# Kernel optimization log

Measured on AMD Instinct MI355X. Metric: run time of the kernel, lower is better.

The kernel has to match this reference:

```python
import jax, jax.numpy as jnp
import numpy as np

NUM_HEADS = 8


def setup_inputs() -> dict:
    key = jax.random.key(0)
    k1, k2, k3 = jax.random.split(key, 3)
    B, N, C = 4, 2048, 1024
    x = jax.random.normal(k1, (B, N, C), dtype=jnp.float32)
    # torch nn.Linear layout: [out_features, in_features]; scaled for stability
    Wqkv = jax.random.normal(k2, (3 * C, C), dtype=jnp.float32) * (C ** -0.5)
    Wproj = jax.random.normal(k3, (C, C), dtype=jnp.float32) * (C ** -0.5)
    return {"x": x, "Wqkv": Wqkv, "Wproj": Wproj}


def reference(x, Wqkv, Wproj):
    B, N, C = x.shape
    H = NUM_HEADS
    D = C // H
    # fused QKV projection (bias=False per config)
    qkv = jnp.einsum('bnc,oc->bno', x, Wqkv)          # [B, N, 3C]
    qkv = qkv.reshape(B, N, 3, H, D)
    q = jnp.transpose(qkv[:, :, 0], (0, 2, 1, 3))     # [B, H, N, D]
    k = jnp.transpose(qkv[:, :, 1], (0, 2, 1, 3))
    v = jnp.transpose(qkv[:, :, 2], (0, 2, 1, 3))
    scale = 1.0 / jnp.sqrt(jnp.asarray(D, dtype=x.dtype))
    scores = jnp.einsum('bhqd,bhkd->bhqk', q, k) * scale
    attn = jax.nn.softmax(scores, axis=-1)            # attn_drop is identity (p=0)
    out = jnp.einsum('bhqk,bhkd->bhqd', attn, v)      # [B, H, N, D]
    out = jnp.transpose(out, (0, 2, 1, 3)).reshape(B, N, C)
    out = jnp.einsum('bnc,oc->bno', out, Wproj)       # proj_drop is identity (p=0)
    return out
```

## Files before the change

### kernel.cpp

```cpp
#include <hip/hip_runtime.h>
#include <hip/hip_bf16.h>
#include <stdint.h>


typedef __bf16 bf16x8 __attribute__((ext_vector_type(8)));
typedef float  f32x4  __attribute__((ext_vector_type(4)));
typedef float  f32x16 __attribute__((ext_vector_type(16)));
typedef short  s16x8  __attribute__((ext_vector_type(8)));
typedef unsigned int u32x4 __attribute__((ext_vector_type(4)));

__device__ __forceinline__ f32x4 mfma_bf16(s16x8 a, s16x8 b, f32x4 c) {
  return __builtin_amdgcn_mfma_f32_16x16x32_bf16(
      __builtin_bit_cast(bf16x8, a), __builtin_bit_cast(bf16x8, b), c, 0, 0, 0);
}

__device__ __forceinline__ f32x16 mfma32(s16x8 a, s16x8 b, f32x16 c) {
  return __builtin_amdgcn_mfma_f32_32x32x16_bf16(
      __builtin_bit_cast(bf16x8, a), __builtin_bit_cast(bf16x8, b), c, 0, 0, 0);
}

__device__ __forceinline__ unsigned short f2bf(float f) {
  unsigned u = __float_as_uint(f);
  u = u + 0x7FFFu + ((u >> 16) & 1u);
  return (unsigned short)(u >> 16);
}

__device__ __forceinline__ unsigned cvt_pk_bf16(float lo, float hi) {
  unsigned r;
  asm("v_cvt_pk_bf16_f32 %0, %1, %2" : "=v"(r) : "v"(lo), "v"(hi));
  return r;
}

__device__ __forceinline__ void load_lds16(const void* g, void* l) {
  __builtin_amdgcn_global_load_lds(
      (const __attribute__((address_space(1))) void*)g,
      (__attribute__((address_space(3))) void*)l, 16, 0, 0);
}


__global__ void cast_kernel(const float* __restrict__ in,
                            unsigned short* __restrict__ out, int n4) {
  int i = blockIdx.x * blockDim.x + threadIdx.x;
  int stride = gridDim.x * blockDim.x;
  for (; i < n4; i += stride) {
    float4 v = reinterpret_cast<const float4*>(in)[i];
    ushort4 o;
    o.x = f2bf(v.x); o.y = f2bf(v.y); o.z = f2bf(v.z); o.w = f2bf(v.w);
    reinterpret_cast<ushort4*>(out)[i] = o;
  }
}


template <bool OUT_BF16>
__global__ __launch_bounds__(256)
void gemm_bt(const short* __restrict__ A, const short* __restrict__ Bw,
             void* __restrict__ Cp, int M, int N, int K) {
  __shared__ __align__(16) short lds_a[4096];
  __shared__ __align__(16) short lds_b[4096];

  const int nbn = N >> 7;
  const int mb  = blockIdx.x / nbn;
  const int nb  = blockIdx.x % nbn;
  const int tid = threadIdx.x;
  const int w   = tid >> 6, l = tid & 63;
  const int lg  = l >> 4, ll = l & 15;
  const int wm  = w >> 1, wn = w & 1;

  f32x4 acc[4][4];
#pragma unroll
  for (int i = 0; i < 4; ++i)
#pragma unroll
    for (int j = 0; j < 4; ++j) acc[i][j] = {0.f, 0.f, 0.f, 0.f};

  const int KT = K >> 5;
  for (int kt = 0; kt < KT; ++kt) {
#pragma unroll
    for (int cc = 0; cc < 4; ++cc) {
      int chunk = w * 4 + cc;
      int c8    = chunk & 7;
      int row   = c8 * 16 + (l >> 2);
      int sg    = (l & 3) ^ (row & 3);
      if (chunk < 8) {
        const short* src = A + (size_t)(mb * 128 + row) * K + kt * 32 + sg * 8;
        load_lds16(src, lds_a + c8 * 512);
      } else {
        const short* src = Bw + (size_t)(nb * 128 + row) * K + kt * 32 + sg * 8;
        load_lds16(src, lds_b + c8 * 512);
      }
    }
    __syncthreads();

    s16x8 af[4], bf[4];
#pragma unroll
    for (int mi = 0; mi < 4; ++mi) {
      int row  = wm * 64 + mi * 16 + ll;
      int slot = lg ^ (row & 3);
      af[mi] = *reinterpret_cast<const s16x8*>(lds_a + row * 32 + slot * 8);
    }
#pragma unroll
    for (int nj = 0; nj < 4; ++nj) {
      int row  = wn * 64 + nj * 16 + ll;
      int slot = lg ^ (row & 3);
      bf[nj] = *reinterpret_cast<const s16x8*>(lds_b + row * 32 + slot * 8);
    }
#pragma unroll
    for (int mi = 0; mi < 4; ++mi)
#pragma unroll
      for (int nj = 0; nj < 4; ++nj)
        acc[mi][nj] = mfma_bf16(af[mi], bf[nj], acc[mi][nj]);
    __syncthreads();
  }

#pragma unroll
  for (int mi = 0; mi < 4; ++mi) {
#pragma unroll
    for (int i = 0; i < 4; ++i) {
      size_t row = (size_t)(mb * 128 + wm * 64 + mi * 16 + lg * 4 + i);
#pragma unroll
      for (int nj = 0; nj < 4; ++nj) {
        int col = nb * 128 + wn * 64 + nj * 16 + ll;
        if (OUT_BF16)
          ((unsigned short*)Cp)[row * N + col] = f2bf(acc[mi][nj][i]);
        else
          ((float*)Cp)[row * N + col] = acc[mi][nj][i];
      }
    }
  }
}


__global__ __launch_bounds__(512, 2)
void attn_fwd(const short* __restrict__ qkv, unsigned short* __restrict__ aout) {
  __shared__ __align__(16) short k_lds[2][64 * 128];
  __shared__ __align__(16) short v_lds[2][128 * 64];

  const int bh = blockIdx.x >> 3;
  const int qb = blockIdx.x & 7;
  const int b = bh >> 3, h = bh & 7;
  const int tid = threadIdx.x;
  const int w = tid >> 6, l = tid & 63;
  const int col = l & 31, hi = l >> 5;

  const size_t base = (size_t)b * 2048 * 3072 + (size_t)h * 128;
  const int qrow0 = qb * 256 + w * 32;

  s16x8 qf[8];
  {
    const short* qp = qkv + base + (size_t)(qrow0 + col) * 3072 + hi * 8;
#pragma unroll
    for (int ks = 0; ks < 8; ++ks)
      qf[ks] = *reinterpret_cast<const s16x8*>(qp + ks * 16);
  }

  f32x16 oacc[4];
#pragma unroll
  for (int nt = 0; nt < 4; ++nt)
#pragma unroll
    for (int r = 0; r < 16; ++r) oacc[nt][r] = 0.f;
  float M = -1e30f, L = 0.f;
  const float csc = 0.08838834764831845f * 1.4426950408889634f;

  s16x8 vr0a, vr0b, vr1a, vr1b;
  const int vr_r0 = (tid & 31) * 2;
  const int vr_c0 = ((tid >> 5) & 7) * 16;

  auto stage_k = [&](int kb, int bf) {
    int wk = w - 4;
#pragma unroll
    for (int cc = 0; cc < 4; ++cc) {
      int c = wk * 4 + cc;
      int row = c * 4 + (l >> 4);
      int sd = (l & 15) ^ (row & 7);
      load_lds16(qkv + base + 1024 + (size_t)(kb * 64 + row) * 3072 + sd * 8,
                 &k_lds[bf][c * 512]);
    }
  };
  auto load_v = [&](int kb) {
    const short* g = qkv + base + 2048 + (size_t)(kb * 64 + vr_r0) * 3072 + vr_c0;
    vr0a = *reinterpret_cast<const s16x8*>(g);
    vr0b = *reinterpret_cast<const s16x8*>(g + 8);
    vr1a = *reinterpret_cast<const s16x8*>(g + 3072);
    vr1b = *reinterpret_cast<const s16x8*>(g + 3072 + 8);
  };
  auto write_v = [&](int bf) {
    char* vbase = reinterpret_cast<char*>(v_lds[bf]);
#pragma unroll
    for (int j = 0; j < 16; ++j) {
      int d = vr_c0 + j;
      unsigned e0 = (unsigned short)(j < 8 ? vr0a[j] : vr0b[j - 8]);
      unsigned e1 = (unsigned short)(j < 8 ? vr1a[j] : vr1b[j - 8]);
      int byte = d * 128 + ((((vr_r0 * 2) >> 4) ^ (d & 7)) << 4) + ((vr_r0 * 2) & 15);
      *reinterpret_cast<unsigned*>(vbase + byte) = e0 | (e1 << 16);
    }
  };

  if (w >= 4) stage_k(0, 0);
  else { load_v(0); write_v(0); }
  __syncthreads();

  for (int kb = 0; kb < 32; ++kb) {
    const int bf = kb & 1;
    if (kb < 31) {
      if (w >= 4) stage_k(kb + 1, bf ^ 1);
      else load_v(kb + 1);
    }

    f32x16 st[2];
#pragma unroll
    for (int kt = 0; kt < 2; ++kt)
#pragma unroll
      for (int r = 0; r < 16; ++r) st[kt][r] = 0.f;
    const char* kbase = reinterpret_cast<const char*>(k_lds[bf]);
#pragma unroll
    for (int ks = 0; ks < 8; ++ks) {
#pragma unroll
      for (int kt = 0; kt < 2; ++kt) {
        int krow = kt * 32 + col;
        int slot = (ks * 2 + hi) ^ (krow & 7);
        s16x8 ak = *reinterpret_cast<const s16x8*>(kbase + krow * 256 + slot * 16);
        st[kt] = mfma32(ak, qf[ks], st[kt]);
      }
    }

    float pm = st[0][0];
#pragma unroll
    for (int r = 1; r < 16; ++r) pm = fmaxf(pm, st[0][r]);
#pragma unroll
    for (int r = 0; r < 16; ++r) pm = fmaxf(pm, st[1][r]);
    pm *= csc;
    pm = fmaxf(pm, __shfl_xor(pm, 32));
    if (!__all(pm <= M + 8.0f)) {
      float Mn = fmaxf(M, pm);
      float f = exp2f(M - Mn);
      M = Mn; L *= f;
#pragma unroll
      for (int r = 0; r < 16; ++r) {
        float fr = __shfl(f, (r & 3) + 8 * (r >> 2) + 4 * hi);
#pragma unroll
        for (int nt = 0; nt < 4; ++nt) oacc[nt][r] *= fr;
      }
    }
    float rs = 0.f;
#pragma unroll
    for (int kt = 0; kt < 2; ++kt)
#pragma unroll
      for (int r = 0; r < 16; ++r) {
        float e = exp2f(fmaf(st[kt][r], csc, -M));
        st[kt][r] = e;
        rs += e;
      }
    rs += __shfl_xor(rs, 32);
    L += rs;

    unsigned wd[16], pw[16];
#pragma unroll
    for (int i = 0; i < 8; ++i) {
      wd[i]     = cvt_pk_bf16(st[0][2 * i], st[0][2 * i + 1]);
      wd[8 + i] = cvt_pk_bf16(st[1][2 * i], st[1][2 * i + 1]);
    }
#pragma unroll
    for (int i = 0; i < 16; ++i) pw[i] = __shfl_xor(wd[i], 32);
    s16x8 pa[4];
#pragma unroll
    for (int kt = 0; kt < 2; ++kt) {
      int bq = kt * 8;
      u32x4 f0 = {hi ? pw[bq + 2] : wd[bq + 0], hi ? pw[bq + 3] : wd[bq + 1],
                  hi ? wd[bq + 2] : pw[bq + 0], hi ? wd[bq + 3] : pw[bq + 1]};
      u32x4 f1 = {hi ? pw[bq + 6] : wd[bq + 4], hi ? pw[bq + 7] : wd[bq + 5],
                  hi ? wd[bq + 6] : pw[bq + 4], hi ? wd[bq + 7] : pw[bq + 5]};
      pa[kt * 2 + 0] = __builtin_bit_cast(s16x8, f0);
      pa[kt * 2 + 1] = __builtin_bit_cast(s16x8, f1);
    }

    const char* vbase = reinterpret_cast<const char*>(v_lds[bf]);
#pragma unroll
    for (int ks = 0; ks < 4; ++ks) {
#pragma unroll
      for (int nt = 0; nt < 4; ++nt) {
        int d = nt * 32 + col;
        int slot = (ks * 2 + hi) ^ (d & 7);
        s16x8 bv = *reinterpret_cast<const s16x8*>(vbase + d * 128 + slot * 16);
        oacc[nt] = mfma32(pa[ks], bv, oacc[nt]);
      }
    }

    if (kb < 31 && w < 4) write_v(bf ^ 1);
    __syncthreads();
  }

  float invl = 1.f / L;
#pragma unroll
  for (int r = 0; r < 16; ++r) {
    int qr = (r & 3) + 8 * (r >> 2) + 4 * hi;
    float il = __shfl(invl, qr);
    size_t row = (size_t)b * 2048 + qrow0 + qr;
#pragma unroll
    for (int nt = 0; nt < 4; ++nt)
      aout[row * 1024 + h * 128 + nt * 32 + col] = f2bf(oacc[nt][r] * il);
  }
}


extern "C" void kernel_launch(void* const* d_in, const int* in_sizes, int n_in,
                              void* d_out, int out_size, void* d_ws, size_t ws_size,
                              hipStream_t stream) {
  const float* x     = (const float*)d_in[0];
  const float* wqkv  = (const float*)d_in[1];
  const float* wproj = (const float*)d_in[2];
  float* out = (float*)d_out;

  char* ws = (char*)d_ws;
  short* xb     = (short*)(ws);
  short* wqkvb  = (short*)(ws + 16777216);
  short* wprojb = (short*)(ws + 23068672);
  short* qkvb   = (short*)(ws + 25165824);
  short* aoutb  = (short*)(ws + 75497472);

  cast_kernel<<<2048, 256, 0, stream>>>(x,     (unsigned short*)xb,     8388608 / 4);
  cast_kernel<<<768,  256, 0, stream>>>(wqkv,  (unsigned short*)wqkvb,  3145728 / 4);
  cast_kernel<<<256,  256, 0, stream>>>(wproj, (unsigned short*)wprojb, 1048576 / 4);

  gemm_bt<true><<<64 * 24, 256, 0, stream>>>(xb, wqkvb, (void*)qkvb, 8192, 3072, 1024);

  attn_fwd<<<32 * 8, 512, 0, stream>>>(qkvb, (unsigned short*)aoutb);

  gemm_bt<false><<<64 * 8, 256, 0, stream>>>(aoutb, wprojb, (void*)out, 8192, 1024, 1024);
}
```

Baseline: 279.9 us.

## Replace GEMMs with 256x256 double-buffered pipelined kernel, fuse casts, add setprio

Replaces the 128x128 single-buffer GEMM with a 256x256-tile, 512-thread kernel. It double-buffers LDS in 64-wide K steps, splits each step into phased prefetch and MFMA blocks with explicit waitcnts and barriers, and remaps blocks with an XCD-aware swizzle. The three cast kernels are merged into one launch, and s_setprio is raised around the MFMA loops in attention. The GEMMs get more reuse per loaded tile and overlap loads with math. In exchange, far fewer workgroups are launched (128 for the projection GEMM on a 256-CU part), which risks underfilling the GPU.

```diff
diff --git a/kernel.cpp b/kernel.cpp
--- a/kernel.cpp
+++ b/kernel.cpp
@@ -38,94 +38,127 @@
 }
 
 
-__global__ void cast_kernel(const float* __restrict__ in,
-                            unsigned short* __restrict__ out, int n4) {
+__global__ void cast3_kernel(const float* __restrict__ x, const float* __restrict__ wq,
+                             const float* __restrict__ wp,
+                             unsigned short* __restrict__ xb,
+                             unsigned short* __restrict__ wqb,
+                             unsigned short* __restrict__ wpb) {
   int i = blockIdx.x * blockDim.x + threadIdx.x;
   int stride = gridDim.x * blockDim.x;
-  for (; i < n4; i += stride) {
-    float4 v = reinterpret_cast<const float4*>(in)[i];
+  for (; i < 3145728; i += stride) {
+    const float4* src; ushort4* dst; int j;
+    if (i < 2097152)      { src = (const float4*)x;  dst = (ushort4*)xb;  j = i; }
+    else if (i < 2883584) { src = (const float4*)wq; dst = (ushort4*)wqb; j = i - 2097152; }
+    else                  { src = (const float4*)wp; dst = (ushort4*)wpb; j = i - 2883584; }
+    float4 v = src[j];
     ushort4 o;
     o.x = f2bf(v.x); o.y = f2bf(v.y); o.z = f2bf(v.z); o.w = f2bf(v.w);
-    reinterpret_cast<ushort4*>(out)[i] = o;
+    dst[j] = o;
   }
 }
 
 
 template <bool OUT_BF16>
-__global__ __launch_bounds__(256)
-void gemm_bt(const short* __restrict__ A, const short* __restrict__ Bw,
+__global__ __launch_bounds__(512, 2)
+void gemm256(const short* __restrict__ A, const short* __restrict__ Bw,
              void* __restrict__ Cp, int M, int N, int K) {
-  __shared__ __align__(16) short lds_a[4096];
-  __shared__ __align__(16) short lds_b[4096];
-
-  const int nbn = N >> 7;
-  const int mb  = blockIdx.x / nbn;
-  const int nb  = blockIdx.x % nbn;
+  __shared__ __align__(16) short a_lds[2][256 * 64];
+  __shared__ __align__(16) short b_lds[2][256 * 64];
+
+  const int nbn = N >> 8;
+  const int nwg = gridDim.x;
+  const int q8 = nwg >> 3;
+  const int swz = (blockIdx.x & 7) * q8 + (blockIdx.x >> 3);
+  const int mb = swz / nbn, nb = swz % nbn;
+
   const int tid = threadIdx.x;
-  const int w   = tid >> 6, l = tid & 63;
-  const int lg  = l >> 4, ll = l & 15;
-  const int wm  = w >> 1, wn = w & 1;
-
-  f32x4 acc[4][4];
-#pragma unroll
-  for (int i = 0; i < 4; ++i)
+  const int w = tid >> 6, l = tid & 63;
+  const int lg = l >> 4, ll = l & 15;
+  const int wm = w >> 2, wn = w & 3;
+
+  f32x4 acc[8][4];
+#pragma unroll
+  for (int i = 0; i < 8; ++i)
 #pragma unroll
     for (int j = 0; j < 4; ++j) acc[i][j] = {0.f, 0.f, 0.f, 0.f};
 
-  const int KT = K >> 5;
-  for (int kt = 0; kt < KT; ++kt) {
-#pragma unroll
-    for (int cc = 0; cc < 4; ++cc) {
-      int chunk = w * 4 + cc;
-      int c8    = chunk & 7;
-      int row   = c8 * 16 + (l >> 2);
-      int sg    = (l & 3) ^ (row & 3);
-      if (chunk < 8) {
-        const short* src = A + (size_t)(mb * 128 + row) * K + kt * 32 + sg * 8;
-        load_lds16(src, lds_a + c8 * 512);
-      } else {
-        const short* src = Bw + (size_t)(nb * 128 + row) * K + kt * 32 + sg * 8;
-        load_lds16(src, lds_b + c8 * 512);
-      }
-    }
-    __syncthreads();
-
-    s16x8 af[4], bf[4];
-#pragma unroll
-    for (int mi = 0; mi < 4; ++mi) {
-      int row  = wm * 64 + mi * 16 + ll;
-      int slot = lg ^ (row & 3);
-      af[mi] = *reinterpret_cast<const s16x8*>(lds_a + row * 32 + slot * 8);
-    }
-#pragma unroll
-    for (int nj = 0; nj < 4; ++nj) {
-      int row  = wn * 64 + nj * 16 + ll;
-      int slot = lg ^ (row & 3);
-      bf[nj] = *reinterpret_cast<const s16x8*>(lds_b + row * 32 + slot * 8);
-    }
+  const int NT = K >> 6;
+
+  auto stage = [&](int t, int g) {
+    short* lptr = (g < 2) ? b_lds[t & 1] : a_lds[t & 1];
+    const short* gp = (g < 2) ? Bw : A;
+    const int gg = g & 1;
+#pragma unroll
+    for (int j = 0; j < 2; ++j) {
+      int r0 = gg * 128 + w * 16 + j * 8;
+      int rl = r0 + (l >> 3);
+      int grow;
+      if (g < 2) grow = nb * 256 + rl;
+      else       grow = mb * 256 + ((rl >> 6) & 1) * 128 + (rl >> 7) * 64 + (rl & 63);
+      const short* src = gp + (size_t)grow * K + t * 64 + (((l & 7) ^ (l >> 3)) << 3);
+      load_lds16(src, lptr + r0 * 64);
+    }
+  };
+
+#define GQ_PHASE(QM, KK, GG, ...)                                              \
+  {                                                                            \
+    const short* ab = a_lds[cur];                                              \
+    const short* bb = b_lds[cur];                                              \
+    const int slot = (((KK) * 4 + lg) ^ (ll & 7)) * 8;                         \
+    s16x8 af[4], bfr[4];                                                       \
+    _Pragma("unroll") for (int mi = 0; mi < 4; ++mi)                           \
+      af[mi] = *reinterpret_cast<const s16x8*>(                                \
+          ab + ((QM) * 128 + wm * 64 + mi * 16 + ll) * 64 + slot);             \
+    _Pragma("unroll") for (int nj = 0; nj < 4; ++nj)                           \
+      bfr[nj] = *reinterpret_cast<const s16x8*>(                               \
+          bb + (wn * 64 + nj * 16 + ll) * 64 + slot);                          \
+    if (pf) stage(t + 1, (GG));                                                \
+    __builtin_amdgcn_s_barrier();                                              \
+    asm volatile("s_waitcnt lgkmcnt(0)" ::: "memory");                         \
+    __builtin_amdgcn_sched_barrier(0);                                         \
+    __builtin_amdgcn_s_setprio(1);                                             \
+    _Pragma("unroll") for (int mi = 0; mi < 4; ++mi)                           \
+      _Pragma("unroll") for (int nj = 0; nj < 4; ++nj)                         \
+        acc[(QM) * 4 + mi][nj] = mfma_bf16(af[mi], bfr[nj], acc[(QM) * 4 + mi][nj]); \
+    __builtin_amdgcn_s_setprio(0);                                             \
+    __VA_ARGS__                                                                \
+    __builtin_amdgcn_s_barrier();                                              \
+  }
+
+  stage(0, 0); stage(0, 1); stage(0, 2); stage(0, 3);
+  asm volatile("s_waitcnt vmcnt(2)" ::: "memory");
+  __builtin_amdgcn_s_barrier();
+
+  for (int t = 0; t < NT; ++t) {
+    const int cur = t & 1;
+    const bool pf = (t + 1 < NT);
+    GQ_PHASE(0, 0, 0, )
+    GQ_PHASE(0, 1, 1,
+      if (pf) { asm volatile("s_waitcnt vmcnt(4)" ::: "memory"); }
+      else    { asm volatile("s_waitcnt vmcnt(0)" ::: "memory"); })
+    GQ_PHASE(1, 0, 2, )
+    GQ_PHASE(1, 1, 3,
+      if (pf) { asm volatile("s_waitcnt vmcnt(2)" ::: "memory"); }
+      else    { asm volatile("s_waitcnt vmcnt(0)" ::: "memory"); })
+  }
+#undef GQ_PHASE
+
+#pragma unroll
+  for (int qm = 0; qm < 2; ++qm)
 #pragma unroll
     for (int mi = 0; mi < 4; ++mi)
 #pragma unroll
-      for (int nj = 0; nj < 4; ++nj)
-        acc[mi][nj] = mfma_bf16(af[mi], bf[nj], acc[mi][nj]);
-    __syncthreads();
-  }
-
-#pragma unroll
-  for (int mi = 0; mi < 4; ++mi) {
-#pragma unroll
-    for (int i = 0; i < 4; ++i) {
-      size_t row = (size_t)(mb * 128 + wm * 64 + mi * 16 + lg * 4 + i);
-#pragma unroll
-      for (int nj = 0; nj < 4; ++nj) {
-        int col = nb * 128 + wn * 64 + nj * 16 + ll;
-        if (OUT_BF16)
-          ((unsigned short*)Cp)[row * N + col] = f2bf(acc[mi][nj][i]);
-        else
-          ((float*)Cp)[row * N + col] = acc[mi][nj][i];
-      }
-    }
-  }
+      for (int i = 0; i < 4; ++i) {
+        size_t row = (size_t)(mb * 256 + wm * 128 + qm * 64 + mi * 16 + lg * 4 + i);
+#pragma unroll
+        for (int nj = 0; nj < 4; ++nj) {
+          int col = nb * 256 + wn * 64 + nj * 16 + ll;
+          if (OUT_BF16)
+            ((unsigned short*)Cp)[row * N + col] = f2bf(acc[qm * 4 + mi][nj][i]);
+          else
+            ((float*)Cp)[row * N + col] = acc[qm * 4 + mi][nj][i];
+        }
+      }
 }
 
 
@@ -211,6 +244,7 @@
 #pragma unroll
       for (int r = 0; r < 16; ++r) st[kt][r] = 0.f;
     const char* kbase = reinterpret_cast<const char*>(k_lds[bf]);
+    __builtin_amdgcn_s_setprio(1);
 #pragma unroll
     for (int ks = 0; ks < 8; ++ks) {
 #pragma unroll
@@ -221,6 +255,7 @@
         st[kt] = mfma32(ak, qf[ks], st[kt]);
       }
     }
+    __builtin_amdgcn_s_setprio(0);
 
     float pm = st[0][0];
 #pragma unroll
@@ -273,6 +308,7 @@
     }
 
     const char* vbase = reinterpret_cast<const char*>(v_lds[bf]);
+    __builtin_amdgcn_s_setprio(1);
 #pragma unroll
     for (int ks = 0; ks < 4; ++ks) {
 #pragma unroll
@@ -283,6 +319,7 @@
         oacc[nt] = mfma32(pa[ks], bv, oacc[nt]);
       }
     }
+    __builtin_amdgcn_s_setprio(0);
 
     if (kb < 31 && w < 4) write_v(bf ^ 1);
     __syncthreads();
@@ -316,13 +353,12 @@
   short* qkvb   = (short*)(ws + 25165824);
   short* aoutb  = (short*)(ws + 75497472);
 
-  cast_kernel<<<2048, 256, 0, stream>>>(x,     (unsigned short*)xb,     8388608 / 4);
-  cast_kernel<<<768,  256, 0, stream>>>(wqkv,  (unsigned short*)wqkvb,  3145728 / 4);
-  cast_kernel<<<256,  256, 0, stream>>>(wproj, (unsigned short*)wprojb, 1048576 / 4);
-
-  gemm_bt<true><<<64 * 24, 256, 0, stream>>>(xb, wqkvb, (void*)qkvb, 8192, 3072, 1024);
+  cast3_kernel<<<2048, 256, 0, stream>>>(x, wqkv, wproj,
+      (unsigned short*)xb, (unsigned short*)wqkvb, (unsigned short*)wprojb);
+
+  gemm256<true><<<384, 512, 0, stream>>>(xb, wqkvb, (void*)qkvb, 8192, 3072, 1024);
 
   attn_fwd<<<32 * 8, 512, 0, stream>>>(qkvb, (unsigned short*)aoutb);
 
-  gemm_bt<false><<<64 * 8, 256, 0, stream>>>(aoutb, wprojb, (void*)out, 8192, 1024, 1024);
-}
+  gemm256<false><<<128, 512, 0, stream>>>(aoutb, wprojb, (void*)out, 8192, 1024, 1024);
+}
```

After: 285.4 us. No clear change (+1.9%).
